# Kernel tuning notes

Hardware: AMD Instinct MI355X
Metric: run time of the kernel (lower is better)

## Reference

```python
import jax, jax.numpy as jnp
import numpy as np

N, F, T, H, E = 50000, 16, 12, 64, 1600000
OUT = 1


def setup_inputs() -> dict:
    key = jax.random.key(0)
    ks = jax.random.split(key, 14)
    inp = {}
    inp["x"] = jax.random.normal(ks[0], (N, F, T), dtype=jnp.float32)
    inp["edge_index"] = jax.random.randint(ks[1], (2, E), 0, N, dtype=jnp.int32)
    inp["edge_weight"] = jax.random.uniform(ks[2], (E,), dtype=jnp.float32)
    C = F + H  # GCN input channels (x concat hidden)
    s = 0.05
    inp["Wz"] = jax.random.normal(ks[3], (C, H), dtype=jnp.float32) * s
    inp["bz"] = jnp.zeros((H,), dtype=jnp.float32)
    inp["Wr"] = jax.random.normal(ks[4], (C, H), dtype=jnp.float32) * s
    inp["br"] = jnp.zeros((H,), dtype=jnp.float32)
    inp["Wh"] = jax.random.normal(ks[5], (C, H), dtype=jnp.float32) * s
    inp["bh"] = jnp.zeros((H,), dtype=jnp.float32)
    inp["Wa"] = jax.random.normal(ks[6], (H, H), dtype=jnp.float32) * s
    inp["ba"] = jnp.zeros((H,), dtype=jnp.float32)
    inp["cv"] = jax.random.normal(ks[7], (H, 1), dtype=jnp.float32) * s
    inp["Wfc"] = jax.random.normal(ks[8], (H, OUT), dtype=jnp.float32) * s
    inp["bfc"] = jnp.zeros((OUT,), dtype=jnp.float32)
    return inp


def _gcn(xc, W, b, src, dst, ew_norm, self_norm, n):
    # PyG GCNConv: D^{-1/2}(A+I)D^{-1/2} X W + b, with self-loop weight 1
    xw = xc @ W                                   # [N, H]
    msg = xw[src] * ew_norm[:, None]              # [E, H] gather
    agg = jax.ops.segment_sum(msg, dst, num_segments=n)  # scatter-add
    return agg + self_norm[:, None] * xw + b


def reference(x, edge_index, edge_weight, Wz, bz, Wr, br, Wh, bh, Wa, ba, cv, Wfc, bfc):
    n = x.shape[0]
    src, dst = edge_index[0], edge_index[1]
    # symmetric normalization with self-loops (weight 1)
    deg = jax.ops.segment_sum(edge_weight, dst, num_segments=n) + 1.0
    dis = jax.lax.rsqrt(deg)
    ew_norm = dis[src] * edge_weight * dis[dst]
    self_norm = dis * dis

    x_seq = jnp.transpose(x, (2, 0, 1))  # [T, N, F]

    def step(h, x_t):
        xh = jnp.concatenate([x_t, h], axis=1)
        z = jax.nn.sigmoid(_gcn(xh, Wz, bz, src, dst, ew_norm, self_norm, n))
        r = jax.nn.sigmoid(_gcn(xh, Wr, br, src, dst, ew_norm, self_norm, n))
        xrh = jnp.concatenate([x_t, r * h], axis=1)
        hc = jnp.tanh(_gcn(xrh, Wh, bh, src, dst, ew_norm, self_norm, n))
        h_new = z * h + (1.0 - z) * hc
        return h_new, h_new

    h0 = jnp.zeros((n, Wz.shape[1]), dtype=x.dtype)
    _, hs_seq = jax.lax.scan(step, h0, x_seq)      # [T, N, H]

    hs_t = jnp.transpose(hs_seq, (1, 0, 2))        # [N, T, H]
    score = jnp.tanh(hs_t @ Wa + ba)               # [N, T, H]
    align = (score @ cv)[..., 0]                   # [N, T]
    alpha = jax.nn.softmax(align, axis=1)          # softmax over time
    context = jnp.einsum('nt,nth->nh', alpha, hs_t)
    out = context @ Wfc + bfc                      # [N, OUT]
    return out
```

## Files before the change

kernel.cpp:

```cpp
#include <hip/hip_runtime.h>
#include <hip/hip_fp16.h>
#include <math.h>

#define Nn 50000
#define Ff 16
#define Tt 12
#define Hh 64
#define Ee 1600000
#define Cc 80

#define SCAN_NB 98

typedef _Float16 f16x8 __attribute__((ext_vector_type(8)));
typedef float f32x4 __attribute__((ext_vector_type(4)));

static __device__ __forceinline__ float sigmoidf_(float x) { return 1.0f / (1.0f + expf(-x)); }

__global__ void k_deg(const int* __restrict__ ei, const float* __restrict__ ew,
                      unsigned long long* __restrict__ dc) {
  int e = blockIdx.x * blockDim.x + threadIdx.x;
  if (e >= Ee) return;
  int d = ei[Ee + e];
  unsigned long long pk = (1ULL << 42) + (unsigned long long)(ew[e] * 2097152.0f + 0.5f);
  atomicAdd(&dc[d], pk);
}

__global__ void k_dis(const unsigned long long* __restrict__ dc,
                      float* __restrict__ dis, int* __restrict__ cnt) {
  int i = blockIdx.x * blockDim.x + threadIdx.x;
  if (i >= Nn) return;
  unsigned long long v = dc[i];
  cnt[i] = (int)(v >> 42);
  float deg = (float)(v & ((1ULL << 42) - 1)) * (1.0f / 2097152.0f);
  dis[i] = 1.0f / sqrtf(deg + 1.0f);
}

__global__ __launch_bounds__(256) void k_scan1(const int* __restrict__ cnt,
                                               int* __restrict__ bsum) {
  __shared__ int ss[256];
  int b = blockIdx.x, t = threadIdx.x;
  int base = b * 512 + t * 2;
  int s = 0;
  if (base < Nn) s += cnt[base];
  if (base + 1 < Nn) s += cnt[base + 1];
  ss[t] = s;
  __syncthreads();
  for (int off = 128; off > 0; off >>= 1) {
    if (t < off) ss[t] += ss[t + off];
    __syncthreads();
  }
  if (t == 0) bsum[b] = ss[0];
}

__global__ __launch_bounds__(128) void k_scan2(const int* __restrict__ bsum,
                                               int* __restrict__ boff) {
  __shared__ int ss[128];
  int t = threadIdx.x;
  int v = (t < SCAN_NB) ? bsum[t] : 0;
  ss[t] = v;
  __syncthreads();
  for (int off = 1; off < 128; off <<= 1) {
    int u = (t >= off) ? ss[t - off] : 0;
    __syncthreads();
    ss[t] += u;
    __syncthreads();
  }
  if (t < SCAN_NB) boff[t] = ss[t] - v;
}

__global__ __launch_bounds__(256) void k_scan3(const int* __restrict__ cnt,
                                               const int* __restrict__ boff,
                                               int* __restrict__ rp, int* __restrict__ cur) {
  __shared__ int ss[256];
  int b = blockIdx.x, t = threadIdx.x;
  int base = b * 512 + t * 2;
  int c0 = (base < Nn) ? cnt[base] : 0;
  int c1 = (base + 1 < Nn) ? cnt[base + 1] : 0;
  int s = c0 + c1;
  ss[t] = s;
  __syncthreads();
  for (int off = 1; off < 256; off <<= 1) {
    int u = (t >= off) ? ss[t - off] : 0;
    __syncthreads();
    ss[t] += u;
    __syncthreads();
  }
  int run = boff[b] + ss[t] - s;
  if (base < Nn) { rp[base] = run; cur[base] = run; }
  if (base + 1 < Nn) { rp[base + 1] = run + c0; cur[base + 1] = run + c0; }
  if (b == 0 && t == 0) rp[Nn] = Ee;
}

__global__ void k_scatter(const int* __restrict__ ei, const float* __restrict__ ew,
                          const float* __restrict__ dis, int* __restrict__ cur,
                          int2* __restrict__ edge2) {
  int e = blockIdx.x * blockDim.x + threadIdx.x;
  if (e >= Ee) return;
  int s = ei[e];
  int d = ei[Ee + e];
  float w = ew[e] * dis[s] * dis[d];
  int pos = atomicAdd(&cur[d], 1);
  edge2[pos] = make_int2(s, __float_as_int(w));
}

__global__ void k_pack(const int2* __restrict__ edge2, unsigned* __restrict__ edge4) {
  int e = blockIdx.x * blockDim.x + threadIdx.x;
  if (e >= Ee) return;
  int2 v = edge2[e];
  __half wh = __float2half(__int_as_float(v.y));
  edge4[e] = (unsigned)(v.x & 0xFFFF) | ((unsigned)__half_as_ushort(wh) << 16);
}

__global__ void k_cvt_x(const float* __restrict__ x, __half* __restrict__ x16) {
  size_t idx = (size_t)blockIdx.x * blockDim.x + threadIdx.x;
  const size_t total = (size_t)Nn * Ff * Tt;
  if (idx < total) x16[idx] = __float2half(x[idx]);
}

__global__ void k_wfrag(const float* __restrict__ Wz, const float* __restrict__ Wr,
                        const float* __restrict__ Wh, __half* __restrict__ frag) {
  int t = blockIdx.x * 256 + threadIdx.x;
  if (t >= 12 * 3 * 64) return;
  int s = t / 192, rem = t % 192, ks = rem / 64, lane = rem % 64;
  int q = lane >> 4, nl = lane & 15;
  const float* W = (s < 4) ? Wz : (s < 8) ? Wr : Wh;
  int n0 = (s & 3) * 16;
  __half tmp[8];
#pragma unroll
  for (int j = 0; j < 8; j++) {
    int k = ks * 32 + q * 8 + j;
    float v = (k < Cc) ? W[k * Hh + n0 + nl] : 0.f;
    tmp[j] = __float2half(v);
  }
  *(uint4*)(frag + ((size_t)(s * 3 + ks) * 64 + lane) * 8) = *(uint4*)tmp;
}

__global__ void k_wfrag_a(const float* __restrict__ Wa, __half* __restrict__ fragA) {
  int t = blockIdx.x * 256 + threadIdx.x;
  if (t >= 8 * 64) return;
  int s = t >> 6, lane = t & 63;
  int tile = s >> 1, ks = s & 1;
  int q = lane >> 4, m = lane & 15;
  __half tmp[8];
#pragma unroll
  for (int j = 0; j < 8; j++) {
    int k = ks * 32 + q * 8 + j;
    tmp[j] = __float2half(Wa[k * Hh + tile * 16 + m]);
  }
  *(uint4*)(fragA + ((size_t)t) * 8) = *(uint4*)tmp;
}

__global__ __launch_bounds__(256) void k_agg_px(
    const float* __restrict__ x, const __half* __restrict__ x16, __half* __restrict__ Px16,
    const int* __restrict__ rp, const int2* __restrict__ edge2,
    const float* __restrict__ dis) {
  int i = blockIdx.x * 4 + (threadIdx.x >> 6);
  if (i >= Nn) return;
  int lane = threadIdx.x & 63;
  const int R = Ff * Tt;
  const bool act = lane < 48;
  float d = dis[i], sn = d * d;
  float a0 = 0.f, a1 = 0.f, a2 = 0.f, a3 = 0.f;
  if (act) {
    float4 sv = *(const float4*)(x + (size_t)i * R + 4 * lane);
    a0 = sn * sv.x; a1 = sn * sv.y; a2 = sn * sv.z; a3 = sn * sv.w;
  }
  int jb = rp[i], je = rp[i + 1];
  for (int j = jb; j < je; j += 2) {
    int jc1 = min(j + 1, Ee - 1);
    int2 e0 = edge2[j];
    int2 e1 = edge2[jc1];
    float w0 = __int_as_float(e0.y);
    bool v1 = (j + 1 < je);
    float w1 = v1 ? __int_as_float(e1.y) : 0.f;
    int s1 = v1 ? e1.x : i;
    if (act) {
      uint2 g0 = *(const uint2*)(x16 + (size_t)e0.x * R + 4 * lane);
      uint2 g1 = *(const uint2*)(x16 + (size_t)s1 * R + 4 * lane);
      float2 p01 = __half22float2(*reinterpret_cast<const __half2*>(&g0.x));
      float2 p23 = __half22float2(*reinterpret_cast<const __half2*>(&g0.y));
      float2 q01 = __half22float2(*reinterpret_cast<const __half2*>(&g1.x));
      float2 q23 = __half22float2(*reinterpret_cast<const __half2*>(&g1.y));
      a0 = fmaf(w0, p01.x, a0); a1 = fmaf(w0, p01.y, a1);
      a2 = fmaf(w0, p23.x, a2); a3 = fmaf(w0, p23.y, a3);
      a0 = fmaf(w1, q01.x, a0); a1 = fmaf(w1, q01.y, a1);
      a2 = fmaf(w1, q23.x, a2); a3 = fmaf(w1, q23.y, a3);
    }
  }
  if (act) {
#pragma unroll
    for (int k = 0; k < 4; k++) {
      int cch = 4 * lane + k;
      int f = cch / Tt, tt = cch % Tt;
      float val = (k == 0) ? a0 : (k == 1) ? a1 : (k == 2) ? a2 : a3;
      Px16[(size_t)tt * Nn * Ff + (size_t)i * Ff + f] = __float2half(val);
    }
  }
}

static __device__ __forceinline__ void stage_px_zero(
    __half* sX16, const __half* __restrict__ Px16t, int i0, int tid) {
  if (tid < 32) {
    int n = tid >> 1, r = tid & 1;
    *(uint4*)(sX16 + n * 104 + r * 8) =
        *(const uint4*)(Px16t + (size_t)(i0 + n) * Ff + r * 8);
  } else if (tid < 80) {
    int p = tid - 32, n = p / 3, part = p % 3;
    *(uint4*)(sX16 + n * 104 + 80 + part * 8) = make_uint4(0u, 0u, 0u, 0u);
  }
}

static __device__ __forceinline__ void acc8_(const uint4& gv, float wt, float* a) {
  float2 f0 = __half22float2(*reinterpret_cast<const __half2*>(&gv.x));
  float2 f1 = __half22float2(*reinterpret_cast<const __half2*>(&gv.y));
  float2 f2 = __half22float2(*reinterpret_cast<const __half2*>(&gv.z));
  float2 f3 = __half22float2(*reinterpret_cast<const __half2*>(&gv.w));
  a[0] = fmaf(wt, f0.x, a[0]); a[1] = fmaf(wt, f0.y, a[1]);
  a[2] = fmaf(wt, f1.x, a[2]); a[3] = fmaf(wt, f1.y, a[3]);
  a[4] = fmaf(wt, f2.x, a[4]); a[5] = fmaf(wt, f2.y, a[5]);
  a[6] = fmaf(wt, f3.x, a[6]); a[7] = fmaf(wt, f3.y, a[7]);
}

static __device__ __forceinline__ void agg_node_to_lds(
    __half* sX16, int n, int i, int lane,
    const __half* __restrict__ v, const int* __restrict__ rp,
    const unsigned* __restrict__ edge4, const float* __restrict__ dis) {
  int g = lane >> 3;
  int c = lane & 7;
  float d = dis[i], sn = d * d;
  float a[8];
  {
    uint4 gv = *(const uint4*)(v + (size_t)i * Hh + 8 * c);
    float ws = (g == 0) ? sn : 0.f;
    float2 f0 = __half22float2(*reinterpret_cast<const __half2*>(&gv.x));
    float2 f1 = __half22float2(*reinterpret_cast<const __half2*>(&gv.y));
    float2 f2 = __half22float2(*reinterpret_cast<const __half2*>(&gv.z));
    float2 f3 = __half22float2(*reinterpret_cast<const __half2*>(&gv.w));
    a[0] = ws * f0.x; a[1] = ws * f0.y; a[2] = ws * f1.x; a[3] = ws * f1.y;
    a[4] = ws * f2.x; a[5] = ws * f2.y; a[6] = ws * f3.x; a[7] = ws * f3.y;
  }
  int jb = rp[i], je = rp[i + 1];
  const unsigned si = (unsigned)i;
  for (int j0 = jb; j0 < je; j0 += 32) {
    int j1 = j0 + g, j2 = j0 + 8 + g, j3 = j0 + 16 + g, j4 = j0 + 24 + g;
    unsigned e1 = edge4[min(j1, Ee - 1)];
    unsigned e2 = edge4[min(j2, Ee - 1)];
    unsigned e3 = edge4[min(j3, Ee - 1)];
    unsigned e4 = edge4[min(j4, Ee - 1)];
    bool v1 = j1 < je, v2 = j2 < je, v3 = j3 < je, v4 = j4 < je;
    float w1 = v1 ? __half2float(__ushort_as_half((unsigned short)(e1 >> 16))) : 0.f;
    float w2 = v2 ? __half2float(__ushort_as_half((unsigned short)(e2 >> 16))) : 0.f;
    float w3 = v3 ? __half2float(__ushort_as_half((unsigned short)(e3 >> 16))) : 0.f;
    float w4 = v4 ? __half2float(__ushort_as_half((unsigned short)(e4 >> 16))) : 0.f;
    unsigned s1 = v1 ? (e1 & 0xFFFFu) : si;
    unsigned s2 = v2 ? (e2 & 0xFFFFu) : si;
    unsigned s3 = v3 ? (e3 & 0xFFFFu) : si;
    unsigned s4 = v4 ? (e4 & 0xFFFFu) : si;
    uint4 g1 = *(const uint4*)(v + (size_t)s1 * Hh + 8 * c);
    uint4 g2 = *(const uint4*)(v + (size_t)s2 * Hh + 8 * c);
    uint4 g3 = *(const uint4*)(v + (size_t)s3 * Hh + 8 * c);
    uint4 g4 = *(const uint4*)(v + (size_t)s4 * Hh + 8 * c);
    acc8_(g1, w1, a);
    acc8_(g2, w2, a);
    acc8_(g3, w3, a);
    acc8_(g4, w4, a);
  }
#pragma unroll
  for (int k2 = 0; k2 < 8; k2++) {
    a[k2] += __shfl_xor(a[k2], 8, 64);
    a[k2] += __shfl_xor(a[k2], 16, 64);
    a[k2] += __shfl_xor(a[k2], 32, 64);
  }
  if (g == 0) {
    __half2 h0 = __floats2half2_rn(a[0], a[1]);
    __half2 h1 = __floats2half2_rn(a[2], a[3]);
    __half2 h2 = __floats2half2_rn(a[4], a[5]);
    __half2 h3 = __floats2half2_rn(a[6], a[7]);
    uint4 st;
    st.x = *reinterpret_cast<unsigned int*>(&h0);
    st.y = *reinterpret_cast<unsigned int*>(&h1);
    st.z = *reinterpret_cast<unsigned int*>(&h2);
    st.w = *reinterpret_cast<unsigned int*>(&h3);
    *(uint4*)(sX16 + n * 104 + 16 + 8 * c) = st;
  }
}

__global__ __launch_bounds__(256) void k_zr_f(
    const __half* __restrict__ Px16, const __half* __restrict__ h16,
    const __half* __restrict__ frag,
    const float* __restrict__ bz, const float* __restrict__ br,
    const int* __restrict__ rp, const unsigned* __restrict__ edge4,
    const float* __restrict__ dis,
    __half* __restrict__ zb16, __half* __restrict__ rh16, int tstep) {
  __shared__ __align__(16) __half sX16[16 * 104];
  const int tid = threadIdx.x;
  const int i0 = blockIdx.x * 16;
  const int wv = tid >> 6, lane = tid & 63;
  stage_px_zero(sX16, Px16 + (size_t)tstep * Nn * Ff, i0, tid);
#pragma unroll
  for (int k = 0; k < 4; k++) {
    int n = wv * 4 + k;
    agg_node_to_lds(sX16, n, i0 + n, lane, h16, rp, edge4, dis);
  }
  __syncthreads();
  f16x8 bzf[3], brf[3];
#pragma unroll
  for (int ks = 0; ks < 3; ks++) {
    bzf[ks] = *(const f16x8*)(frag + ((size_t)(wv * 3 + ks) * 64 + lane) * 8);
    brf[ks] = *(const f16x8*)(frag + ((size_t)((4 + wv) * 3 + ks) * 64 + lane) * 8);
  }
  const int m = lane & 15, q = lane >> 4;
  f32x4 accz = {0.f, 0.f, 0.f, 0.f}, accr = {0.f, 0.f, 0.f, 0.f};
#pragma unroll
  for (int ks = 0; ks < 3; ks++) {
    f16x8 a = *(const f16x8*)(sX16 + m * 104 + ks * 32 + q * 8);
    accz = __builtin_amdgcn_mfma_f32_16x16x32_f16(a, bzf[ks], accz, 0, 0, 0);
    accr = __builtin_amdgcn_mfma_f32_16x16x32_f16(a, brf[ks], accr, 0, 0, 0);
  }
  const int o = wv * 16 + m;
  float bzo = bz[o], bro = br[o];
  const int nb = i0 + q * 4;
#pragma unroll
  for (int r = 0; r < 4; r++) {
    int node = nb + r;
    float zv = sigmoidf_(accz[r] + bzo);
    float rv = sigmoidf_(accr[r] + bro);
    float hv = __half2float(h16[(size_t)node * Hh + o]);
    zb16[(size_t)node * Hh + o] = __float2half(zv);
    rh16[(size_t)node * Hh + o] = __float2half(rv * hv);
  }
}

__global__ __launch_bounds__(256) void k_h_f(
    const __half* __restrict__ Px16, const __half* __restrict__ rh16,
    const __half* __restrict__ zb16, float* __restrict__ h, __half* __restrict__ h16,
    __half* __restrict__ hs16, const __half* __restrict__ frag,
    const float* __restrict__ bh,
    const int* __restrict__ rp, const unsigned* __restrict__ edge4,
    const float* __restrict__ dis, int tstep) {
  __shared__ __align__(16) __half sX16[16 * 104];
  const int tid = threadIdx.x;
  const int i0 = blockIdx.x * 16;
  const int wv = tid >> 6, lane = tid & 63;
  stage_px_zero(sX16, Px16 + (size_t)tstep * Nn * Ff, i0, tid);
#pragma unroll
  for (int k = 0; k < 4; k++) {
    int n = wv * 4 + k;
    agg_node_to_lds(sX16, n, i0 + n, lane, rh16, rp, edge4, dis);
  }
  __syncthreads();
  f16x8 bf[3];
#pragma unroll
  for (int ks = 0; ks < 3; ks++)
    bf[ks] = *(const f16x8*)(frag + ((size_t)((8 + wv) * 3 + ks) * 64 + lane) * 8);
  const int m = lane & 15, q = lane >> 4;
  f32x4 acc = {0.f, 0.f, 0.f, 0.f};
#pragma unroll
  for (int ks = 0; ks < 3; ks++) {
    f16x8 a = *(const f16x8*)(sX16 + m * 104 + ks * 32 + q * 8);
    acc = __builtin_amdgcn_mfma_f32_16x16x32_f16(a, bf[ks], acc, 0, 0, 0);
  }
  const int o = wv * 16 + m;
  float bho = bh[o];
  const int nb = i0 + q * 4;
  __half* hst = hs16 + (size_t)tstep * Nn * Hh;
#pragma unroll
  for (int r = 0; r < 4; r++) {
    int node = nb + r;
    float hc = tanhf(acc[r] + bho);
    float zv = __half2float(zb16[(size_t)node * Hh + o]);
    float hv = h[(size_t)node * Hh + o];
    float hn = zv * hv + (1.0f - zv) * hc;
    h[(size_t)node * Hh + o] = hn;
    __half hh = __float2half(hn);
    h16[(size_t)node * Hh + o] = hh;
    hst[(size_t)node * Hh + o] = hh;
  }
}

__global__ __launch_bounds__(256) void k_att(
    const __half* __restrict__ hs16, const __half* __restrict__ fragA,
    const float* __restrict__ ba, const float* __restrict__ cv,
    const float* __restrict__ Wfc, const float* __restrict__ bfc,
    float* __restrict__ out) {
  const int tid = threadIdx.x;
  const int wv = tid >> 6, lane = tid & 63;
  const int i = blockIdx.x * 4 + wv;
  if (i >= Nn) return;
  const int m = lane & 15, q = lane >> 4;

  f16x8 bf[4][2];
#pragma unroll
  for (int s = 0; s < 8; s++)
    bf[s >> 1][s & 1] = *(const f16x8*)(fragA + (size_t)(s * 64 + lane) * 8);

  const int tm = (m < Tt) ? m : (Tt - 1);
  const __half* hbase = hs16 + (size_t)tm * Nn * Hh + (size_t)i * Hh;
  f16x8 a0 = *(const f16x8*)(hbase + q * 8);
  f16x8 a1 = *(const f16x8*)(hbase + 32 + q * 8);

  f32x4 acc[4];
#pragma unroll
  for (int tile = 0; tile < 4; tile++) acc[tile] = f32x4{0.f, 0.f, 0.f, 0.f};
#pragma unroll
  for (int tile = 0; tile < 4; tile++) {
    acc[tile] = __builtin_amdgcn_mfma_f32_16x16x32_f16(a0, bf[tile][0], acc[tile], 0, 0, 0);
    acc[tile] = __builtin_amdgcn_mfma_f32_16x16x32_f16(a1, bf[tile][1], acc[tile], 0, 0, 0);
  }

  float ba_l[4], cv_l[4];
#pragma unroll
  for (int tile = 0; tile < 4; tile++) {
    ba_l[tile] = ba[tile * 16 + m];
    cv_l[tile] = cv[tile * 16 + m];
  }
  float ar[4];
#pragma unroll
  for (int r = 0; r < 4; r++) {
    float s = 0.f;
#pragma unroll
    for (int tile = 0; tile < 4; tile++)
      s += tanhf(acc[tile][r] + ba_l[tile]) * cv_l[tile];
    s += __shfl_xor(s, 1, 64);
    s += __shfl_xor(s, 2, 64);
    s += __shfl_xor(s, 4, 64);
    s += __shfl_xor(s, 8, 64);
    ar[r] = s;
  }
  float al[Tt];
#pragma unroll
  for (int t = 0; t < Tt; t++) al[t] = __shfl(ar[t & 3], (t >> 2) * 16, 64);
  float mx = al[0];
#pragma unroll
  for (int t = 1; t < Tt; t++) mx = fmaxf(mx, al[t]);
  float ssum = 0.f;
#pragma unroll
  for (int t = 0; t < Tt; t++) { al[t] = expf(al[t] - mx); ssum += al[t]; }
  float inv = 1.0f / ssum;
  float cx = 0.f;
#pragma unroll
  for (int t = 0; t < Tt; t++)
    cx = fmaf(al[t], __half2float(hs16[(size_t)t * Nn * Hh + (size_t)i * Hh + lane]), cx);
  float p = cx * inv * Wfc[lane];
#pragma unroll
  for (int off = 32; off >= 1; off >>= 1) p += __shfl_xor(p, off, 64);
  if (lane == 0) out[i] = p + bfc[0];
}

extern "C" void kernel_launch(void* const* d_in, const int* in_sizes, int n_in,
                              void* d_out, int out_size, void* d_ws, size_t ws_size,
                              hipStream_t stream) {
  const float* x   = (const float*)d_in[0];
  const int* ei    = (const int*)d_in[1];
  const float* ew  = (const float*)d_in[2];
  const float* Wz  = (const float*)d_in[3];
  const float* bz  = (const float*)d_in[4];
  const float* Wr  = (const float*)d_in[5];
  const float* br  = (const float*)d_in[6];
  const float* Wh  = (const float*)d_in[7];
  const float* bh  = (const float*)d_in[8];
  const float* Wa  = (const float*)d_in[9];
  const float* ba  = (const float*)d_in[10];
  const float* cv  = (const float*)d_in[11];
  const float* Wfc = (const float*)d_in[12];
  const float* bfc = (const float*)d_in[13];
  float* out = (float*)d_out;

  char* w = (char*)d_ws;
  auto alloc = [&](size_t bytes) {
    char* p = w;
    w += (bytes + 255) & ~(size_t)255;
    return p;
  };
  unsigned long long* dc = (unsigned long long*)alloc((size_t)Nn * 8);
  float* dis = (float*)alloc((size_t)Nn * 4);
  int* cnt   = (int*)alloc((size_t)Nn * 4);
  int* rp    = (int*)alloc((size_t)(Nn + 1) * 4);
  int* cur   = (int*)alloc((size_t)Nn * 4);
  int* bsum  = (int*)alloc((size_t)SCAN_NB * 4);
  int* boff  = (int*)alloc((size_t)SCAN_NB * 4);
  int2* edge2 = (int2*)alloc((size_t)Ee * 8);
  unsigned* edge4 = (unsigned*)alloc((size_t)Ee * 4);
  __half* x16  = (__half*)alloc((size_t)Nn * Ff * Tt * 2);
  __half* Px16 = (__half*)alloc((size_t)Tt * Nn * Ff * 2);
  float* h     = (float*)alloc((size_t)Nn * Hh * 4);
  __half* h16  = (__half*)alloc((size_t)Nn * Hh * 2);
  __half* rh16 = (__half*)alloc((size_t)Nn * Hh * 2);
  __half* zb16 = (__half*)alloc((size_t)Nn * Hh * 2);
  __half* hs16 = (__half*)alloc((size_t)Tt * Nn * Hh * 2);
  __half* wfrag = (__half*)alloc((size_t)12 * 3 * 64 * 8 * 2);
  __half* wfragA = (__half*)alloc((size_t)8 * 64 * 8 * 2);

  hipMemsetAsync(dc, 0, (size_t)Nn * 8, stream);
  hipMemsetAsync(h, 0, (size_t)Nn * Hh * 4, stream);
  hipMemsetAsync(h16, 0, (size_t)Nn * Hh * 2, stream);

  k_deg<<<(Ee + 255) / 256, 256, 0, stream>>>(ei, ew, dc);
  k_dis<<<(Nn + 255) / 256, 256, 0, stream>>>(dc, dis, cnt);
  k_scan1<<<SCAN_NB, 256, 0, stream>>>(cnt, bsum);
  k_scan2<<<1, 128, 0, stream>>>(bsum, boff);
  k_scan3<<<SCAN_NB, 256, 0, stream>>>(cnt, boff, rp, cur);
  k_scatter<<<(Ee + 255) / 256, 256, 0, stream>>>(ei, ew, dis, cur, edge2);
  k_pack<<<(Ee + 255) / 256, 256, 0, stream>>>(edge2, edge4);
  {
    const size_t total = (size_t)Nn * Ff * Tt;
    k_cvt_x<<<(int)((total + 255) / 256), 256, 0, stream>>>(x, x16);
  }
  k_wfrag<<<9, 256, 0, stream>>>(Wz, Wr, Wh, wfrag);
  k_wfrag_a<<<2, 256, 0, stream>>>(Wa, wfragA);
  k_agg_px<<<(Nn + 3) / 4, 256, 0, stream>>>(x, x16, Px16, rp, edge2, dis);

  const int gGemm = Nn / 16;
  const int gNode = (Nn + 3) / 4;
  for (int t = 0; t < Tt; t++) {
    k_zr_f<<<gGemm, 256, 0, stream>>>(Px16, h16, wfrag, bz, br, rp, edge4, dis,
                                      zb16, rh16, t);
    k_h_f<<<gGemm, 256, 0, stream>>>(Px16, rh16, zb16, h, h16, hs16, wfrag, bh,
                                     rp, edge4, dis, t);
  }
  k_att<<<gNode, 256, 0, stream>>>(hs16, wfragA, ba, cv, Wfc, bfc, out);
}
```

Before: 1.327 ms.

## Pack edges directly in scatter and store hidden history node-major

The scatter kernel now writes the packed 16-bit-source/fp16-weight edge word directly, which removes the 8-byte int2 edge array and the separate pack pass. The x-aggregation kernel reads the packed form instead. The hidden-state history buffer changes from time-major to node-major, so the attention kernel reads each node's 12 timesteps from one contiguous span. In exchange, the recurrent kernel's per-step history writes become strided, and the aggregation pass now uses fp16 edge weights.

Result: no change. 1.320 ms (-0.5%).

```diff
diff --git a/kernel.cpp b/kernel.cpp
--- a/kernel.cpp
+++ b/kernel.cpp
@@ -93,22 +93,15 @@
 
 __global__ void k_scatter(const int* __restrict__ ei, const float* __restrict__ ew,
                           const float* __restrict__ dis, int* __restrict__ cur,
-                          int2* __restrict__ edge2) {
+                          unsigned* __restrict__ edge4) {
   int e = blockIdx.x * blockDim.x + threadIdx.x;
   if (e >= Ee) return;
   int s = ei[e];
   int d = ei[Ee + e];
   float w = ew[e] * dis[s] * dis[d];
   int pos = atomicAdd(&cur[d], 1);
-  edge2[pos] = make_int2(s, __float_as_int(w));
-}
-
-__global__ void k_pack(const int2* __restrict__ edge2, unsigned* __restrict__ edge4) {
-  int e = blockIdx.x * blockDim.x + threadIdx.x;
-  if (e >= Ee) return;
-  int2 v = edge2[e];
-  __half wh = __float2half(__int_as_float(v.y));
-  edge4[e] = (unsigned)(v.x & 0xFFFF) | ((unsigned)__half_as_ushort(wh) << 16);
+  __half wh = __float2half(w);
+  edge4[pos] = (unsigned)(s & 0xFFFF) | ((unsigned)__half_as_ushort(wh) << 16);
 }
 
 __global__ void k_cvt_x(const float* __restrict__ x, __half* __restrict__ x16) {
@@ -152,7 +145,7 @@
 
 __global__ __launch_bounds__(256) void k_agg_px(
     const float* __restrict__ x, const __half* __restrict__ x16, __half* __restrict__ Px16,
-    const int* __restrict__ rp, const int2* __restrict__ edge2,
+    const int* __restrict__ rp, const unsigned* __restrict__ edge4,
     const float* __restrict__ dis) {
   int i = blockIdx.x * 4 + (threadIdx.x >> 6);
   if (i >= Nn) return;
@@ -166,16 +159,17 @@
     a0 = sn * sv.x; a1 = sn * sv.y; a2 = sn * sv.z; a3 = sn * sv.w;
   }
   int jb = rp[i], je = rp[i + 1];
+  const unsigned si = (unsigned)i;
   for (int j = jb; j < je; j += 2) {
-    int jc1 = min(j + 1, Ee - 1);
-    int2 e0 = edge2[j];
-    int2 e1 = edge2[jc1];
-    float w0 = __int_as_float(e0.y);
+    unsigned e0 = edge4[j];
+    unsigned e1 = edge4[min(j + 1, Ee - 1)];
+    float w0 = __half2float(__ushort_as_half((unsigned short)(e0 >> 16)));
     bool v1 = (j + 1 < je);
-    float w1 = v1 ? __int_as_float(e1.y) : 0.f;
-    int s1 = v1 ? e1.x : i;
+    float w1 = v1 ? __half2float(__ushort_as_half((unsigned short)(e1 >> 16))) : 0.f;
+    unsigned s0 = e0 & 0xFFFFu;
+    unsigned s1 = v1 ? (e1 & 0xFFFFu) : si;
     if (act) {
-      uint2 g0 = *(const uint2*)(x16 + (size_t)e0.x * R + 4 * lane);
+      uint2 g0 = *(const uint2*)(x16 + (size_t)s0 * R + 4 * lane);
       uint2 g1 = *(const uint2*)(x16 + (size_t)s1 * R + 4 * lane);
       float2 p01 = __half22float2(*reinterpret_cast<const __half2*>(&g0.x));
       float2 p23 = __half22float2(*reinterpret_cast<const __half2*>(&g0.y));
@@ -363,7 +357,6 @@
   const int o = wv * 16 + m;
   float bho = bh[o];
   const int nb = i0 + q * 4;
-  __half* hst = hs16 + (size_t)tstep * Nn * Hh;
 #pragma unroll
   for (int r = 0; r < 4; r++) {
     int node = nb + r;
@@ -374,7 +367,7 @@
     h[(size_t)node * Hh + o] = hn;
     __half hh = __float2half(hn);
     h16[(size_t)node * Hh + o] = hh;
-    hst[(size_t)node * Hh + o] = hh;
+    hs16[(size_t)node * (Tt * Hh) + tstep * Hh + o] = hh;
   }
 }
 
@@ -395,7 +388,7 @@
     bf[s >> 1][s & 1] = *(const f16x8*)(fragA + (size_t)(s * 64 + lane) * 8);
 
   const int tm = (m < Tt) ? m : (Tt - 1);
-  const __half* hbase = hs16 + (size_t)tm * Nn * Hh + (size_t)i * Hh;
+  const __half* hbase = hs16 + (size_t)i * (Tt * Hh) + tm * Hh;
   f16x8 a0 = *(const f16x8*)(hbase + q * 8);
   f16x8 a1 = *(const f16x8*)(hbase + 32 + q * 8);
 
@@ -440,7 +433,7 @@
   float cx = 0.f;
 #pragma unroll
   for (int t = 0; t < Tt; t++)
-    cx = fmaf(al[t], __half2float(hs16[(size_t)t * Nn * Hh + (size_t)i * Hh + lane]), cx);
+    cx = fmaf(al[t], __half2float(hs16[(size_t)i * (Tt * Hh) + t * Hh + lane]), cx);
   float p = cx * inv * Wfc[lane];
 #pragma unroll
   for (int off = 32; off >= 1; off >>= 1) p += __shfl_xor(p, off, 64);
@@ -479,7 +472,6 @@
   int* cur   = (int*)alloc((size_t)Nn * 4);
   int* bsum  = (int*)alloc((size_t)SCAN_NB * 4);
   int* boff  = (int*)alloc((size_t)SCAN_NB * 4);
-  int2* edge2 = (int2*)alloc((size_t)Ee * 8);
   unsigned* edge4 = (unsigned*)alloc((size_t)Ee * 4);
   __half* x16  = (__half*)alloc((size_t)Nn * Ff * Tt * 2);
   __half* Px16 = (__half*)alloc((size_t)Tt * Nn * Ff * 2);
@@ -487,7 +479,7 @@
   __half* h16  = (__half*)alloc((size_t)Nn * Hh * 2);
   __half* rh16 = (__half*)alloc((size_t)Nn * Hh * 2);
   __half* zb16 = (__half*)alloc((size_t)Nn * Hh * 2);
-  __half* hs16 = (__half*)alloc((size_t)Tt * Nn * Hh * 2);
+  __half* hs16 = (__half*)alloc((size_t)Nn * Tt * Hh * 2);
   __half* wfrag = (__half*)alloc((size_t)12 * 3 * 64 * 8 * 2);
   __half* wfragA = (__half*)alloc((size_t)8 * 64 * 8 * 2);
 
@@ -500,15 +492,14 @@
   k_scan1<<<SCAN_NB, 256, 0, stream>>>(cnt, bsum);
   k_scan2<<<1, 128, 0, stream>>>(bsum, boff);
   k_scan3<<<SCAN_NB, 256, 0, stream>>>(cnt, boff, rp, cur);
-  k_scatter<<<(Ee + 255) / 256, 256, 0, stream>>>(ei, ew, dis, cur, edge2);
-  k_pack<<<(Ee + 255) / 256, 256, 0, stream>>>(edge2, edge4);
+  k_scatter<<<(Ee + 255) / 256, 256, 0, stream>>>(ei, ew, dis, cur, edge4);
   {
     const size_t total = (size_t)Nn * Ff * Tt;
     k_cvt_x<<<(int)((total + 255) / 256), 256, 0, stream>>>(x, x16);
   }
   k_wfrag<<<9, 256, 0, stream>>>(Wz, Wr, Wh, wfrag);
   k_wfrag_a<<<2, 256, 0, stream>>>(Wa, wfragA);
-  k_agg_px<<<(Nn + 3) / 4, 256, 0, stream>>>(x, x16, Px16, rp, edge2, dis);
+  k_agg_px<<<(Nn + 3) / 4, 256, 0, stream>>>(x, x16, Px16, rp, edge4, dis);
 
   const int gGemm = Nn / 16;
   const int gNode = (Nn + 3) / 4;
```
